# Performance work log

Measured on AMD Instinct MI355X. Metric: run time of the kernel, lower is better.

## Reference

```python
import jax, jax.numpy as jnp
import numpy as np

S = 7
B = 2
CLS = 20
N = CLS + B * 5  # 30
LAMBDA_COORD = 5.0
LAMBDA_NOOBJ = 0.5
BATCH = 16384


def setup_inputs() -> dict:
    key = jax.random.key(0)
    k1, k2, k3 = jax.random.split(key, 3)
    pred = jax.random.uniform(k1, (BATCH, S, S, N), dtype=jnp.float32)
    target = jax.random.uniform(k2, (BATCH, S, S, N), dtype=jnp.float32)
    # conf channel (index 4) must be exactly 0 or 1 -- it drives the obj/noobj masks
    obj = (jax.random.uniform(k3, (BATCH, S, S)) < 0.15).astype(jnp.float32)
    target = target.at[..., 4].set(obj)
    return {"pred": pred, "target": target}


def _iou(b1, b2):
    # b1: [M, B, 4] xyxy, b2: [M, 4] xyxy -> [M, B]
    lt = jnp.maximum(b1[..., :2], b2[:, None, :2])
    rb = jnp.minimum(b1[..., 2:], b2[:, None, 2:])
    wh = jnp.clip(rb - lt, 0.0)
    inter = wh[..., 0] * wh[..., 1]
    area1 = (b1[..., 2] - b1[..., 0]) * (b1[..., 3] - b1[..., 1])
    area2 = ((b2[:, 2] - b2[:, 0]) * (b2[:, 3] - b2[:, 1]))[:, None]
    union = area1 + area2 - inter
    return jnp.where(union > 0, inter / union, 0.0)


def reference(pred, target):
    batch = pred.shape[0]
    p = pred.reshape(-1, N)   # [M, 30], M = batch*S*S
    t = target.reshape(-1, N)
    obj = (t[:, 4] == 1).astype(pred.dtype)    # positive-cell mask
    noobj = (t[:, 4] == 0).astype(pred.dtype)  # negative-cell mask

    # faithful to source: conf_loc = arange(B)*B + 4 -> [4, 6]
    conf_loc = jnp.arange(B) * B + 4
    noobj_conf_loss = jnp.sum(noobj[:, None] * (p[:, conf_loc] - t[:, conf_loc]) ** 2)

    pb = p[:, : B * 5].reshape(-1, B, 5)  # [M, B, 5] (x, y, w, h, conf)
    tb = t[:, :5]                         # [M, 5] first target box per cell

    # xywh -> xyxy
    pb_xyxy = jnp.concatenate([pb[..., :2] - pb[..., 2:4] / 2,
                               pb[..., :2] + pb[..., 2:4] / 2], axis=-1)
    tb_xyxy = jnp.concatenate([tb[:, :2] - tb[:, 2:4] / 2,
                               tb[:, :2] + tb[:, 2:4] / 2], axis=-1)

    iou = _iou(pb_xyxy, tb_xyxy)                         # [M, B]
    j = jnp.argmax(iou, axis=1)                          # responsible box index
    max_iou = jax.lax.stop_gradient(jnp.max(iou, axis=1))
    resp = jnp.take_along_axis(pb, j[:, None, None], axis=1)[:, 0]  # [M, 5]

    xy_loss = jnp.sum((resp[:, :2] - tb[:, :2]) ** 2, axis=-1)
    wh_loss = jnp.sum((jnp.sqrt(jnp.clip(resp[:, 2:4], 0.0))
                       - jnp.sqrt(jnp.clip(tb[:, 2:4], 0.0))) ** 2, axis=-1)
    coord_loss = jnp.sum(obj * (xy_loss + wh_loss))

    obj_conf_loss = jnp.sum(obj * (resp[:, 4] - max_iou) ** 2)
    class_loss = jnp.sum(obj[:, None] * (p[:, B * 5:] - t[:, B * 5:]) ** 2)

    total = (LAMBDA_COORD * coord_loss + obj_conf_loss
             + LAMBDA_NOOBJ * noobj_conf_loss + class_loss) / batch
    return total
```

## Files before the change

kernel.cpp:

```cpp
#include <hip/hip_runtime.h>


#define TPB 64
#define CPC 128
#define CB  (CPC * 120)
#define NCALLS (CB / 1024)
#define R_TOTAL (16384 * 7 * 7)
#define NCHUNKS (R_TOTAL / CPC)
#define GRID 512

__device__ __forceinline__ void gload_lds16(const void* g, void* l) {
    __builtin_amdgcn_global_load_lds(
        (const __attribute__((address_space(1))) void*)g,
        (__attribute__((address_space(3))) void*)l, 16, 0, 0);
}

__global__ __launch_bounds__(TPB) void yolo_loss_kernel(
    const float* __restrict__ pred, const float* __restrict__ target,
    float* __restrict__ out)
{
    __shared__ __align__(16) unsigned char smem[2][2 * CB];

    const int lane = threadIdx.x;
    float sum = 0.0f;

    {
        const char* gp = (const char*)pred + (size_t)blockIdx.x * CB + lane * 16;
        const char* gt = (const char*)target + (size_t)blockIdx.x * CB + lane * 16;
        #pragma unroll
        for (int c = 0; c < NCALLS; c++) gload_lds16(gp + c * 1024, &smem[0][c * 1024]);
        #pragma unroll
        for (int c = 0; c < NCALLS; c++) gload_lds16(gt + c * 1024, &smem[0][CB + c * 1024]);
    }

    int buf = 0;
    for (size_t chunk = blockIdx.x; chunk < NCHUNKS; chunk += GRID) {
        const size_t next = chunk + GRID;
        if (next < NCHUNKS) {
            const char* gp = (const char*)pred + next * CB + lane * 16;
            const char* gt = (const char*)target + next * CB + lane * 16;
            unsigned char* lb = smem[buf ^ 1];
            #pragma unroll
            for (int c = 0; c < NCALLS; c++) gload_lds16(gp + c * 1024, lb + c * 1024);
            #pragma unroll
            for (int c = 0; c < NCALLS; c++) gload_lds16(gt + c * 1024, lb + CB + c * 1024);
            asm volatile("s_waitcnt vmcnt(30)" ::: "memory");
        } else {
            asm volatile("s_waitcnt vmcnt(0)" ::: "memory");
        }

        const unsigned char* lb = smem[buf];
        #pragma unroll
        for (int half = 0; half < 2; half++) {
            const int cell = lane + half * 64;
            const float* pf = (const float*)(lb + cell * 120);
            const float* tf = (const float*)(lb + CB + cell * 120);

            const float t4 = tf[4];
            if (t4 == 0.0f) {
                float d4 = pf[4] - t4;
                float d6 = pf[6] - tf[6];
                sum += 0.5f * (d4 * d4 + d6 * d6);
            } else if (t4 == 1.0f) {
                float tx1 = tf[0] - tf[2] * 0.5f, ty1 = tf[1] - tf[3] * 0.5f;
                float tx2 = tf[0] + tf[2] * 0.5f, ty2 = tf[1] + tf[3] * 0.5f;
                float area2 = (tx2 - tx1) * (ty2 - ty1);

                float ax1 = pf[0] - pf[2] * 0.5f, ay1 = pf[1] - pf[3] * 0.5f;
                float ax2 = pf[0] + pf[2] * 0.5f, ay2 = pf[1] + pf[3] * 0.5f;
                float w0 = fmaxf(fminf(ax2, tx2) - fmaxf(ax1, tx1), 0.0f);
                float h0 = fmaxf(fminf(ay2, ty2) - fmaxf(ay1, ty1), 0.0f);
                float inter0 = w0 * h0;
                float uni0 = (ax2 - ax1) * (ay2 - ay1) + area2 - inter0;
                float iou0 = (uni0 > 0.0f) ? (inter0 / uni0) : 0.0f;

                float bx1 = pf[5] - pf[7] * 0.5f, by1 = pf[6] - pf[8] * 0.5f;
                float bx2 = pf[5] + pf[7] * 0.5f, by2 = pf[6] + pf[8] * 0.5f;
                float w1 = fmaxf(fminf(bx2, tx2) - fmaxf(bx1, tx1), 0.0f);
                float h1 = fmaxf(fminf(by2, ty2) - fmaxf(by1, ty1), 0.0f);
                float inter1 = w1 * h1;
                float uni1 = (bx2 - bx1) * (by2 - by1) + area2 - inter1;
                float iou1 = (uni1 > 0.0f) ? (inter1 / uni1) : 0.0f;

                bool j1 = (iou1 > iou0);
                float max_iou = fmaxf(iou0, iou1);
                float r0 = j1 ? pf[5] : pf[0];
                float r1 = j1 ? pf[6] : pf[1];
                float r2 = j1 ? pf[7] : pf[2];
                float r3 = j1 ? pf[8] : pf[3];
                float r4 = j1 ? pf[9] : pf[4];

                float dx = r0 - tf[0];
                float dy = r1 - tf[1];
                float sw = sqrtf(fmaxf(r2, 0.0f)) - sqrtf(fmaxf(tf[2], 0.0f));
                float sh = sqrtf(fmaxf(r3, 0.0f)) - sqrtf(fmaxf(tf[3], 0.0f));
                float coord = dx * dx + dy * dy + sw * sw + sh * sh;
                float dc = r4 - max_iou;

                float cls = 0.0f;
                #pragma unroll
                for (int k = 10; k < 30; k++) {
                    float d = pf[k] - tf[k];
                    cls += d * d;
                }
                sum += 5.0f * coord + dc * dc + cls;
            }
        }
        buf ^= 1;
    }

    #pragma unroll
    for (int off = 32; off > 0; off >>= 1)
        sum += __shfl_down(sum, off, 64);
    if (lane == 0)
        atomicAdd(out, sum * (1.0f / 16384.0f));
}

extern "C" void kernel_launch(void* const* d_in, const int* in_sizes, int n_in,
                              void* d_out, int out_size, void* d_ws, size_t ws_size,
                              hipStream_t stream) {
    const float* pred = (const float*)d_in[0];
    const float* target = (const float*)d_in[1];
    float* out = (float*)d_out;
    hipMemsetAsync(out, 0, sizeof(float), stream);
    yolo_loss_kernel<<<GRID, TPB, 0, stream>>>(pred, target, out);
}
```

Measured before the change: 207.0 us.

## Replace persistent double-buffered LDS DMA loop with one-tile-per-block register staging

Drops the persistent 512-block kernel that double-buffered chunks through LDS with direct global-to-LDS loads. Instead it launches one 256-thread block per 256 cells, loads each tile with coalesced float4/float2 loads into registers, writes them to LDS, syncs, and has each thread handle one cell. A block-level reduction through a small shared array cuts atomics to one per block. The aim is more memory-level parallelism from many resident blocks in place of manual pipelining. The cost is 3136 atomics and an extra register-to-LDS copy.

```diff
diff --git a/kernel.cpp b/kernel.cpp
--- a/kernel.cpp
+++ b/kernel.cpp
@@ -1,119 +1,103 @@
 #include <hip/hip_runtime.h>
 
 
-#define TPB 64
-#define CPC 128
-#define CB  (CPC * 120)
-#define NCALLS (CB / 1024)
-#define R_TOTAL (16384 * 7 * 7)
-#define NCHUNKS (R_TOTAL / CPC)
-#define GRID 512
+#define TPB 256
+#define CELLS 256
+#define CB 30720
+#define GRID 3136
 
-__device__ __forceinline__ void gload_lds16(const void* g, void* l) {
-    __builtin_amdgcn_global_load_lds(
-        (const __attribute__((address_space(1))) void*)g,
-        (__attribute__((address_space(3))) void*)l, 16, 0, 0);
-}
-
-__global__ __launch_bounds__(TPB) void yolo_loss_kernel(
+__global__ __launch_bounds__(TPB, 2) void yolo_loss_kernel(
     const float* __restrict__ pred, const float* __restrict__ target,
     float* __restrict__ out)
 {
-    __shared__ __align__(16) unsigned char smem[2][2 * CB];
+    __shared__ __align__(16) unsigned char smem[2 * CB];
+    __shared__ float red[TPB / 64];
 
-    const int lane = threadIdx.x;
+    const int tid = threadIdx.x;
+    const size_t base = (size_t)blockIdx.x * CB;
+
+    const char* gp = (const char*)pred + base;
+    const char* gt = (const char*)target + base;
+    float4 vp[7], vt[7];
+    float2 wp, wt;
+    #pragma unroll
+    for (int i = 0; i < 7; i++) vp[i] = *(const float4*)(gp + i * 4096 + tid * 16);
+    wp = *(const float2*)(gp + 28672 + tid * 8);
+    #pragma unroll
+    for (int i = 0; i < 7; i++) vt[i] = *(const float4*)(gt + i * 4096 + tid * 16);
+    wt = *(const float2*)(gt + 28672 + tid * 8);
+
+    #pragma unroll
+    for (int i = 0; i < 7; i++) *(float4*)(smem + i * 4096 + tid * 16) = vp[i];
+    *(float2*)(smem + 28672 + tid * 8) = wp;
+    #pragma unroll
+    for (int i = 0; i < 7; i++) *(float4*)(smem + CB + i * 4096 + tid * 16) = vt[i];
+    *(float2*)(smem + CB + 28672 + tid * 8) = wt;
+    __syncthreads();
+
+    const float* pf = (const float*)(smem) + tid * 30;
+    const float* tf = (const float*)(smem + CB) + tid * 30;
+
     float sum = 0.0f;
+    const float t4 = tf[4];
+    if (t4 == 0.0f) {
+        float d4 = pf[4] - t4;
+        float d6 = pf[6] - tf[6];
+        sum = 0.5f * (d4 * d4 + d6 * d6);
+    } else if (t4 == 1.0f) {
+        float tx1 = tf[0] - tf[2] * 0.5f, ty1 = tf[1] - tf[3] * 0.5f;
+        float tx2 = tf[0] + tf[2] * 0.5f, ty2 = tf[1] + tf[3] * 0.5f;
+        float area2 = (tx2 - tx1) * (ty2 - ty1);
 
-    {
-        const char* gp = (const char*)pred + (size_t)blockIdx.x * CB + lane * 16;
-        const char* gt = (const char*)target + (size_t)blockIdx.x * CB + lane * 16;
+        float ax1 = pf[0] - pf[2] * 0.5f, ay1 = pf[1] - pf[3] * 0.5f;
+        float ax2 = pf[0] + pf[2] * 0.5f, ay2 = pf[1] + pf[3] * 0.5f;
+        float w0 = fmaxf(fminf(ax2, tx2) - fmaxf(ax1, tx1), 0.0f);
+        float h0 = fmaxf(fminf(ay2, ty2) - fmaxf(ay1, ty1), 0.0f);
+        float inter0 = w0 * h0;
+        float uni0 = (ax2 - ax1) * (ay2 - ay1) + area2 - inter0;
+        float iou0 = (uni0 > 0.0f) ? (inter0 / uni0) : 0.0f;
+
+        float bx1 = pf[5] - pf[7] * 0.5f, by1 = pf[6] - pf[8] * 0.5f;
+        float bx2 = pf[5] + pf[7] * 0.5f, by2 = pf[6] + pf[8] * 0.5f;
+        float w1 = fmaxf(fminf(bx2, tx2) - fmaxf(bx1, tx1), 0.0f);
+        float h1 = fmaxf(fminf(by2, ty2) - fmaxf(by1, ty1), 0.0f);
+        float inter1 = w1 * h1;
+        float uni1 = (bx2 - bx1) * (by2 - by1) + area2 - inter1;
+        float iou1 = (uni1 > 0.0f) ? (inter1 / uni1) : 0.0f;
+
+        bool j1 = (iou1 > iou0);
+        float max_iou = fmaxf(iou0, iou1);
+        float r0 = j1 ? pf[5] : pf[0];
+        float r1 = j1 ? pf[6] : pf[1];
+        float r2 = j1 ? pf[7] : pf[2];
+        float r3 = j1 ? pf[8] : pf[3];
+        float r4 = j1 ? pf[9] : pf[4];
+
+        float dx = r0 - tf[0];
+        float dy = r1 - tf[1];
+        float sw = sqrtf(fmaxf(r2, 0.0f)) - sqrtf(fmaxf(tf[2], 0.0f));
+        float sh = sqrtf(fmaxf(r3, 0.0f)) - sqrtf(fmaxf(tf[3], 0.0f));
+        float coord = dx * dx + dy * dy + sw * sw + sh * sh;
+        float dc = r4 - max_iou;
+
+        float cls = 0.0f;
         #pragma unroll
-        for (int c = 0; c < NCALLS; c++) gload_lds16(gp + c * 1024, &smem[0][c * 1024]);
-        #pragma unroll
-        for (int c = 0; c < NCALLS; c++) gload_lds16(gt + c * 1024, &smem[0][CB + c * 1024]);
-    }
-
-    int buf = 0;
-    for (size_t chunk = blockIdx.x; chunk < NCHUNKS; chunk += GRID) {
-        const size_t next = chunk + GRID;
-        if (next < NCHUNKS) {
-            const char* gp = (const char*)pred + next * CB + lane * 16;
-            const char* gt = (const char*)target + next * CB + lane * 16;
-            unsigned char* lb = smem[buf ^ 1];
-            #pragma unroll
-            for (int c = 0; c < NCALLS; c++) gload_lds16(gp + c * 1024, lb + c * 1024);
-            #pragma unroll
-            for (int c = 0; c < NCALLS; c++) gload_lds16(gt + c * 1024, lb + CB + c * 1024);
-            asm volatile("s_waitcnt vmcnt(30)" ::: "memory");
-        } else {
-            asm volatile("s_waitcnt vmcnt(0)" ::: "memory");
+        for (int k = 10; k < 30; k++) {
+            float d = pf[k] - tf[k];
+            cls += d * d;
         }
-
-        const unsigned char* lb = smem[buf];
-        #pragma unroll
-        for (int half = 0; half < 2; half++) {
-            const int cell = lane + half * 64;
-            const float* pf = (const float*)(lb + cell * 120);
-            const float* tf = (const float*)(lb + CB + cell * 120);
-
-            const float t4 = tf[4];
-            if (t4 == 0.0f) {
-                float d4 = pf[4] - t4;
-                float d6 = pf[6] - tf[6];
-                sum += 0.5f * (d4 * d4 + d6 * d6);
-            } else if (t4 == 1.0f) {
-                float tx1 = tf[0] - tf[2] * 0.5f, ty1 = tf[1] - tf[3] * 0.5f;
-                float tx2 = tf[0] + tf[2] * 0.5f, ty2 = tf[1] + tf[3] * 0.5f;
-                float area2 = (tx2 - tx1) * (ty2 - ty1);
-
-                float ax1 = pf[0] - pf[2] * 0.5f, ay1 = pf[1] - pf[3] * 0.5f;
-                float ax2 = pf[0] + pf[2] * 0.5f, ay2 = pf[1] + pf[3] * 0.5f;
-                float w0 = fmaxf(fminf(ax2, tx2) - fmaxf(ax1, tx1), 0.0f);
-                float h0 = fmaxf(fminf(ay2, ty2) - fmaxf(ay1, ty1), 0.0f);
-                float inter0 = w0 * h0;
-                float uni0 = (ax2 - ax1) * (ay2 - ay1) + area2 - inter0;
-                float iou0 = (uni0 > 0.0f) ? (inter0 / uni0) : 0.0f;
-
-                float bx1 = pf[5] - pf[7] * 0.5f, by1 = pf[6] - pf[8] * 0.5f;
-                float bx2 = pf[5] + pf[7] * 0.5f, by2 = pf[6] + pf[8] * 0.5f;
-                float w1 = fmaxf(fminf(bx2, tx2) - fmaxf(bx1, tx1), 0.0f);
-                float h1 = fmaxf(fminf(by2, ty2) - fmaxf(by1, ty1), 0.0f);
-                float inter1 = w1 * h1;
-                float uni1 = (bx2 - bx1) * (by2 - by1) + area2 - inter1;
-                float iou1 = (uni1 > 0.0f) ? (inter1 / uni1) : 0.0f;
-
-                bool j1 = (iou1 > iou0);
-                float max_iou = fmaxf(iou0, iou1);
-                float r0 = j1 ? pf[5] : pf[0];
-                float r1 = j1 ? pf[6] : pf[1];
-                float r2 = j1 ? pf[7] : pf[2];
-                float r3 = j1 ? pf[8] : pf[3];
-                float r4 = j1 ? pf[9] : pf[4];
-
-                float dx = r0 - tf[0];
-                float dy = r1 - tf[1];
-                float sw = sqrtf(fmaxf(r2, 0.0f)) - sqrtf(fmaxf(tf[2], 0.0f));
-                float sh = sqrtf(fmaxf(r3, 0.0f)) - sqrtf(fmaxf(tf[3], 0.0f));
-                float coord = dx * dx + dy * dy + sw * sw + sh * sh;
-                float dc = r4 - max_iou;
-
-                float cls = 0.0f;
-                #pragma unroll
-                for (int k = 10; k < 30; k++) {
-                    float d = pf[k] - tf[k];
-                    cls += d * d;
-                }
-                sum += 5.0f * coord + dc * dc + cls;
-            }
-        }
-        buf ^= 1;
+        sum = 5.0f * coord + dc * dc + cls;
     }
 
     #pragma unroll
     for (int off = 32; off > 0; off >>= 1)
         sum += __shfl_down(sum, off, 64);
-    if (lane == 0)
-        atomicAdd(out, sum * (1.0f / 16384.0f));
+    if ((tid & 63) == 0) red[tid >> 6] = sum;
+    __syncthreads();
+    if (tid == 0) {
+        float s = red[0] + red[1] + red[2] + red[3];
+        atomicAdd(out, s * (1.0f / 16384.0f));
+    }
 }
 
 extern "C" void kernel_launch(void* const* d_in, const int* in_sizes, int n_in,
```

Result: no change. 204.2 us (-1.3%).
